# Kernel optimization log

Measured on AMD Instinct MI355X. Metric: run time of the kernel, lower is better.

## Reference

```python
import jax, jax.numpy as jnp
import numpy as np
import math

NUM_BINS = 10
TAIL_BOUND = 5.0
FILTER_CHANNELS = 192
KERNEL_SIZE = 3
N_LAYERS = 3
HALF = 1
MIN_BIN = 1e-3
MIN_DERIV = 1e-3


def conv1d(x, w, b, dilation=1, groups=1, padding=0):
    # x: [B,C,T], w: [O, C//groups, K]
    y = jax.lax.conv_general_dilated(
        x, w, window_strides=(1,), padding=[(padding, padding)],
        rhs_dilation=(dilation,), dimension_numbers=('NCH', 'OIH', 'NCH'),
        feature_group_count=groups)
    return y + b[None, :, None]


def ln_channels(x, g, b, eps=1e-5):
    # LayerNorm over channel dim (VITS modules.LayerNorm)
    m = jnp.mean(x, axis=1, keepdims=True)
    v = jnp.mean((x - m) ** 2, axis=1, keepdims=True)
    return g[None, :, None] * (x - m) * jax.lax.rsqrt(v + eps) + b[None, :, None]


def rq_spline(x1, uw, uh, ud):
    # piecewise rational-quadratic transform with linear tails (Durkan et al.)
    # x1: [B,1,T]; uw,uh: [B,1,T,K]; ud: [B,1,T,K-1]
    K = NUM_BINS
    tb = TAIL_BOUND
    inside = (x1 >= -tb) & (x1 <= tb)

    const = math.log(math.exp(1.0 - MIN_DERIV) - 1.0)  # softplus^-1(1-min_d)
    ud = jnp.pad(ud, [(0, 0)] * (ud.ndim - 1) + [(1, 1)], constant_values=const)

    widths = jax.nn.softmax(uw, axis=-1)
    widths = MIN_BIN + (1.0 - MIN_BIN * K) * widths
    cumw = jnp.pad(jnp.cumsum(widths, -1), [(0, 0)] * (uw.ndim - 1) + [(1, 0)])
    cumw = 2.0 * tb * cumw - tb
    cumw = cumw.at[..., 0].set(-tb).at[..., -1].set(tb)
    widths = cumw[..., 1:] - cumw[..., :-1]

    heights = jax.nn.softmax(uh, axis=-1)
    heights = MIN_BIN + (1.0 - MIN_BIN * K) * heights
    cumh = jnp.pad(jnp.cumsum(heights, -1), [(0, 0)] * (uh.ndim - 1) + [(1, 0)])
    cumh = 2.0 * tb * cumh - tb
    cumh = cumh.at[..., 0].set(-tb).at[..., -1].set(tb)
    heights = cumh[..., 1:] - cumh[..., :-1]

    derivs = MIN_DERIV + jax.nn.softplus(ud)  # [..., K+1]

    xin = jnp.clip(x1, -tb, tb)  # clamp so out-of-range lanes stay finite
    locs = cumw.at[..., -1].add(1e-6)
    bin_idx = jnp.clip(jnp.sum((xin[..., None] >= locs).astype(jnp.int32), -1) - 1, 0, K - 1)

    def take(a):
        return jnp.take_along_axis(a, bin_idx[..., None], axis=-1)[..., 0]

    icw = take(cumw)
    iw = take(widths)
    ich = take(cumh)
    ih = take(heights)
    d_l = take(derivs[..., :-1])
    d_r = take(derivs[..., 1:])
    delta = ih / iw

    theta = (xin - icw) / iw
    t1m = theta * (1.0 - theta)
    numerator = ih * (delta * theta * theta + d_l * t1m)
    denominator = delta + (d_l + d_r - 2.0 * delta) * t1m
    y = ich + numerator / denominator
    dnum = (delta * delta) * (d_r * theta * theta + 2.0 * delta * t1m + d_l * (1.0 - theta) ** 2)
    lad = jnp.log(dnum) - 2.0 * jnp.log(denominator)

    out = jnp.where(inside, y, x1)       # linear tails: identity outside
    lad = jnp.where(inside, lad, 0.0)
    return out, lad


def reference(x, x_mask, pre_w, pre_b, sep_w, sep_b, pw_w, pw_b,
              ln1_g, ln1_b, ln2_g, ln2_b, proj_w, proj_b):
    x0, x1 = x[:, :HALF], x[:, HALF:]
    h = conv1d(x0, pre_w, pre_b)
    # DDSConv (dilated depth-separable conv stack), p_dropout=0
    for i in range(N_LAYERS):
        d = KERNEL_SIZE ** i
        pad = (KERNEL_SIZE * d - d) // 2
        y = conv1d(h * x_mask, sep_w[i], sep_b[i], dilation=d,
                   groups=FILTER_CHANNELS, padding=pad)
        y = jax.nn.gelu(ln_channels(y, ln1_g[i], ln1_b[i]), approximate=False)
        y = conv1d(y, pw_w[i], pw_b[i])
        y = jax.nn.gelu(ln_channels(y, ln2_g[i], ln2_b[i]), approximate=False)
        h = h + y
    h = h * x_mask
    h = conv1d(h, proj_w, proj_b) * x_mask  # [B, half*(3K-1), T]
    b, c, t = x0.shape
    h = h.reshape(b, c, -1, t).transpose(0, 1, 3, 2)  # [B, half, T, 3K-1]
    scale = math.sqrt(FILTER_CHANNELS)
    uw = h[..., :NUM_BINS] / scale
    uh = h[..., NUM_BINS:2 * NUM_BINS] / scale
    ud = h[..., 2 * NUM_BINS:]
    x1o, lad = rq_spline(x1, uw, uh, ud)
    out = jnp.concatenate([x0, x1o], axis=1) * x_mask
    logdet = jnp.sum(lad * x_mask, axis=(1, 2))
    return out, logdet


def setup_inputs() -> dict:
    key = jax.random.key(0)
    ks = jax.random.split(key, 8)
    B, T, C, L, K = 64, 4096, FILTER_CHANNELS, N_LAYERS, KERNEL_SIZE
    return {
        'x': jax.random.normal(ks[0], (B, 2, T), jnp.float32),
        'x_mask': jnp.ones((B, 1, T), jnp.float32),
        'pre_w': jax.random.normal(ks[1], (C, 1, 1), jnp.float32) * 0.1,
        'pre_b': jnp.zeros((C,), jnp.float32),
        'sep_w': jax.random.normal(ks[2], (L, C, 1, K), jnp.float32) * 0.1,
        'sep_b': jnp.zeros((L, C), jnp.float32),
        'pw_w': jax.random.normal(ks[3], (L, C, C, 1), jnp.float32) * (1.0 / np.sqrt(C).astype(np.float32)),
        'pw_b': jnp.zeros((L, C), jnp.float32),
        'ln1_g': jnp.ones((L, C), jnp.float32),
        'ln1_b': jnp.zeros((L, C), jnp.float32),
        'ln2_g': jnp.ones((L, C), jnp.float32),
        'ln2_b': jnp.zeros((L, C), jnp.float32),
        'proj_w': jax.random.normal(ks[4], (HALF * (3 * NUM_BINS - 1), C, 1), jnp.float32) * 0.01,
        'proj_b': jnp.zeros((HALF * (3 * NUM_BINS - 1),), jnp.float32),
    }
```

## Files before the change

kernel.cpp:

```cpp
#include <hip/hip_runtime.h>
#include <stdint.h>

#define TT_ 4096
#define CC_ 192
#define TILE_ 64
#define HALO_ 13
#define TW_ 90
#define HS_ 100
#define YTS_ 200
#define NT_ 512

typedef float f32x2 __attribute__((ext_vector_type(2)));
typedef float f32x4 __attribute__((ext_vector_type(4)));
typedef short s16x4 __attribute__((ext_vector_type(4)));
typedef short s16x8 __attribute__((ext_vector_type(8)));
typedef uint32_t ui32x2 __attribute__((ext_vector_type(2)));
typedef uint32_t ui32x4 __attribute__((ext_vector_type(4)));

__device__ __forceinline__ float bf2f(short s){
  uint32_t u = ((uint32_t)(uint16_t)s) << 16;
  float f; __builtin_memcpy(&f, &u, 4); return f;
}
__device__ __forceinline__ float bfhalf(uint32_t u, int hi){
  uint32_t v = hi ? (u & 0xFFFF0000u) : (u << 16);
  float f; __builtin_memcpy(&f, &v, 4); return f;
}
__device__ __forceinline__ short f2bf(float f){
  uint32_t u; __builtin_memcpy(&u, &f, 4);
  u += 0x7FFFu + ((u >> 16) & 1u);
  return (short)(u >> 16);
}
__device__ __forceinline__ uint32_t fbits(float f){
  uint32_t u; __builtin_memcpy(&u, &f, 4); return u;
}
__device__ __forceinline__ uint32_t pk_trunc(float lo, float hi){
  return __builtin_amdgcn_perm(fbits(hi), fbits(lo), 0x07060302u);
}
__device__ __forceinline__ uint32_t rne_u(float f){
  uint32_t u = fbits(f);
  return u + 0x7FFFu + ((u >> 16) & 1u);
}
__device__ __forceinline__ uint32_t pk_rne(float lo, float hi){
  return __builtin_amdgcn_perm(rne_u(hi), rne_u(lo), 0x07060302u);
}
__device__ __forceinline__ f32x2 pfma(f32x2 a, f32x2 b, f32x2 c){
  return __builtin_elementwise_fma(a, b, c);
}
__device__ __forceinline__ f32x2 gelu2(f32x2 x){
  f32x2 s = x*x;
  f32x2 t = pfma(s, f32x2{0.0713548162f,0.0713548162f}, f32x2{1.5957691216f,1.5957691216f});
  f32x2 p = x*t;
  f32x2 q = p * f32x2{-1.44269504089f,-1.44269504089f};
  f32x2 e; e[0] = __builtin_amdgcn_exp2f(q[0]); e[1] = __builtin_amdgcn_exp2f(q[1]);
  f32x2 d = e + f32x2{1.f,1.f};
  f32x2 r; r[0] = __builtin_amdgcn_rcpf(d[0]); r[1] = __builtin_amdgcn_rcpf(d[1]);
  return x*r;
}
__device__ __forceinline__ int ytix(int row, int col){
  int key = (row ^ (row >> 2)) & 3;
  return row*YTS_ + ((((col >> 3) ^ key) << 3) | (col & 7));
}

template<int D>
__device__ __forceinline__ void dw_pass(const short* __restrict__ Hs, short* __restrict__ YTs,
    const float* __restrict__ sw, const float* __restrict__ sb,
    int jlo, int jhi, int tid){
  constexpr int WO = (D==9) ? 16 : 8;
  constexpr int NU = (D==9) ? 20 : 12;
  for (int g = tid; g < 96*12; g += NT_){
    int cg = g % 96, jg = g / 96;
    int j0 = jg*8;
    if (j0 + 8 <= jlo || j0 >= jhi) continue;
    int c0 = cg*2;
    uint32_t wpa[NU], wpb[NU];
    {
      const uint32_t* ra = (const uint32_t*)(Hs + (c0+0)*HS_ + j0 - WO);
      const uint32_t* rb = (const uint32_t*)(Hs + (c0+1)*HS_ + j0 - WO);
      #pragma unroll
      for (int u = 0; u < NU/2; ++u){
        ui32x2 ta = *(const ui32x2*)(ra + u*2);
        ui32x2 tb = *(const ui32x2*)(rb + u*2);
        wpa[u*2] = ta[0]; wpa[u*2+1] = ta[1];
        wpb[u*2] = tb[0]; wpb[u*2+1] = tb[1];
      }
    }
    f32x2 wv0 = { sw[c0*3+0], sw[c0*3+3] };
    f32x2 wv1 = { sw[c0*3+1], sw[c0*3+4] };
    f32x2 wv2 = { sw[c0*3+2], sw[c0*3+5] };
    f32x2 bb2 = { sb[c0], sb[c0+1] };
    #pragma unroll
    for (int j = 0; j < 8; ++j){
      int h0 = WO + j - D, h1 = WO + j, h2 = WO + j + D;
      f32x2 t0 = { bfhalf(wpa[h0>>1], h0&1), bfhalf(wpb[h0>>1], h0&1) };
      f32x2 t1 = { bfhalf(wpa[h1>>1], h1&1), bfhalf(wpb[h1>>1], h1&1) };
      f32x2 t2 = { bfhalf(wpa[h2>>1], h2&1), bfhalf(wpb[h2>>1], h2&1) };
      f32x2 acc = pfma(wv0, t0, pfma(wv1, t1, pfma(wv2, t2, bb2)));
      *(uint32_t*)(YTs + ytix(j0+j, c0)) = pk_trunc(acc[0], acc[1]);
    }
  }
}

__device__ __forceinline__ void ln_stats(const short* __restrict__ YTs, float* __restrict__ SM,
                                         float* __restrict__ SR, int jlo, int jhi, int tid){
  if (tid < 384){
    int row = tid >> 2, qtr = tid & 3;
    if (row >= jlo && row < jhi){
      f32x2 s2 = {0.f,0.f}, q2 = {0.f,0.f};
      #pragma unroll
      for (int u=0;u<6;++u){
        ui32x4 w = *(const ui32x4*)(YTs + ytix(row, qtr*48 + u*8));
        #pragma unroll
        for (int k=0;k<4;++k){
          f32x2 pr = { bfhalf(w[k],0), bfhalf(w[k],1) };
          s2 += pr; q2 = pfma(pr, pr, q2);
        }
      }
      float s = s2[0]+s2[1], q = q2[0]+q2[1];
      s += __shfl_xor(s,1); q += __shfl_xor(q,1);
      s += __shfl_xor(s,2); q += __shfl_xor(q,2);
      if (qtr==0){
        float mean = s*(1.f/192.f);
        float var = fmaxf(q*(1.f/192.f) - mean*mean, 0.f);
        SM[row]=mean; SR[row]=rsqrtf(var+1e-5f);
      }
    }
  }
}

__global__ __launch_bounds__(512, 4)
void convflow_main(
    const float* __restrict__ x, const float* __restrict__ xmask,
    const float* __restrict__ pre_w, const float* __restrict__ pre_b,
    const float* __restrict__ sep_w, const float* __restrict__ sep_b,
    const float* __restrict__ pw_b,
    const float* __restrict__ ln1_g, const float* __restrict__ ln1_b,
    const float* __restrict__ ln2_g, const float* __restrict__ ln2_b,
    const float* __restrict__ proj_b,
    const short* __restrict__ Wbf, const short* __restrict__ Pbf,
    float* __restrict__ out, float* __restrict__ part)
{
  __shared__ __align__(16) char smem_raw[78592];
  float* MB = (float*)(smem_raw + 0);
  float* XB = (float*)(smem_raw + 640);
  float* SM = (float*)(smem_raw + 1024);
  float* SR = (float*)(smem_raw + 1408);
  short* H  = (short*)(smem_raw + 1792);
  short* YT = (short*)(smem_raw + 40192);
  float* HP = (float*)(smem_raw + 65792);

  const int tid = threadIdx.x;
  const int b = blockIdx.y, tile = blockIdx.x;
  const int t0 = tile*TILE_ - HALO_;

  for (int idx = tid; idx < 160; idx += NT_){
    int j = idx - 16; int t = t0 + j;
    float m = 0.f;
    if (j >= 0 && j < TW_ && t >= 0 && t < TT_) m = xmask[b*TT_ + t];
    MB[idx] = m;
  }
  if (tid < 96){
    int t = t0 + tid; float v = 0.f;
    if (tid < TW_ && t >= 0 && t < TT_) v = x[(b*2)*TT_ + t];
    XB[tid] = v;
  }
  __syncthreads();

  for (int g = tid; g < CC_*24; g += NT_){
    int jq = g % 24, c = g / 24;
    float w = pre_w[c], bb = pre_b[c];
    int j0 = jq*4;
    float v0 = (w*XB[j0+0] + bb)*MB[16+j0+0];
    float v1 = (w*XB[j0+1] + bb)*MB[16+j0+1];
    float v2 = (w*XB[j0+2] + bb)*MB[16+j0+2];
    float v3 = (w*XB[j0+3] + bb)*MB[16+j0+3];
    ui32x2 o; o[0] = pk_rne(v0, v1); o[1] = pk_rne(v2, v3);
    *(ui32x2*)(H + c*HS_ + j0) = o;
  }
  __syncthreads();

  #pragma unroll 1
  for (int li = 0; li < 3; ++li){
    const int jlo = (li==0) ? 1 : ((li==1) ? 4 : 13);
    const int jhi = (li==0) ? 89 : ((li==1) ? 86 : 77);
    const float* sw = sep_w + li*CC_*3;
    const float* sb = sep_b + li*CC_;

    if (li == 0)      dw_pass<1>(H, YT, sw, sb, jlo, jhi, tid);
    else if (li == 1) dw_pass<3>(H, YT, sw, sb, jlo, jhi, tid);
    else              dw_pass<9>(H, YT, sw, sb, jlo, jhi, tid);
    __syncthreads();

    ln_stats(YT, SM, SR, jlo, jhi, tid); __syncthreads();

    {
      const float* g1 = ln1_g + li*CC_;
      const float* b1 = ln1_b + li*CC_;
      for (int g = tid; g < 96*24; g += NT_){
        int ch = g % 24, row = g / 24;
        short* p = YT + ytix(row, ch*8);
        if (row >= jlo && row < jhi){
          float m = SM[row], r = SR[row];
          f32x2 r2 = {r, r}, nm2 = {-m, -m};
          f32x4 ga = *(const f32x4*)&g1[ch*8], gb = *(const f32x4*)&g1[ch*8+4];
          f32x4 ba = *(const f32x4*)&b1[ch*8], bb = *(const f32x4*)&b1[ch*8+4];
          ui32x4 v = *(ui32x4*)p;
          ui32x4 o;
          #pragma unroll
          for (int k=0;k<4;++k){
            f32x2 pr = { bfhalf(v[k],0), bfhalf(v[k],1) };
            f32x2 gk = (k<2) ? f32x2{ga[2*k], ga[2*k+1]} : f32x2{gb[2*k-4], gb[2*k-3]};
            f32x2 bk = (k<2) ? f32x2{ba[2*k], ba[2*k+1]} : f32x2{bb[2*k-4], bb[2*k-3]};
            f32x2 A = gk * r2;
            f32x2 B = pfma(A, nm2, bk);
            f32x2 val = pfma(pr, A, B);
            f32x2 gl = gelu2(val);
            o[k] = pk_trunc(gl[0], gl[1]);
          }
          *(ui32x4*)p = o;
        } else {
          ui32x4 z = {0u,0u,0u,0u};
          *(ui32x4*)p = z;
        }
      }
    }
    __syncthreads();

    {
      int w = tid >> 6, lane = tid & 63, l16 = lane & 15, q = lane >> 4;
      int Mh = w & 3, Nh = w >> 2;
      f32x4 acc[3][3];
      #pragma unroll
      for (int r=0;r<3;r++)
        #pragma unroll
        for (int s=0;s<3;s++){ f32x4 z = {0.f,0.f,0.f,0.f}; acc[r][s] = z; }
      const short* Wl = Wbf + li*CC_*CC_;
      #pragma unroll
      for (int kk=0;kk<6;++kk){
        s16x8 bv[3], av[3];
        #pragma unroll
        for (int s=0;s<3;++s)
          bv[s] = *(const s16x8*)&YT[ytix((Nh*3+s)*16 + l16, kk*32 + q*8)];
        #pragma unroll
        for (int r=0;r<3;++r)
          av[r] = *(const s16x8*)&Wl[((Mh*3+r)*16 + l16)*CC_ + kk*32 + q*8];
        #pragma unroll
        for (int r=0;r<3;++r)
          #pragma unroll
          for (int s=0;s<3;++s)
            acc[r][s] = __builtin_amdgcn_mfma_f32_16x16x32_bf16(av[r], bv[s], acc[r][s], 0, 0, 0);
      }
      __syncthreads();
      #pragma unroll
      for (int r=0;r<3;++r){
        int m0 = (Mh*3+r)*16 + q*4;
        f32x4 bias = *(const f32x4*)&pw_b[li*CC_ + m0];
        #pragma unroll
        for (int s=0;s<3;++s){
          int n = (Nh*3+s)*16 + l16;
          ui32x2 ov;
          ov[0] = pk_trunc(acc[r][s][0]+bias[0], acc[r][s][1]+bias[1]);
          ov[1] = pk_trunc(acc[r][s][2]+bias[2], acc[r][s][3]+bias[3]);
          *(ui32x2*)(YT + ytix(n, m0)) = ov;
        }
      }
      __syncthreads();
    }

    ln_stats(YT, SM, SR, jlo, jhi, tid); __syncthreads();

    {
      const float* g2 = ln2_g + li*CC_;
      const float* b2 = ln2_b + li*CC_;
      for (int g = tid; g < 24*48; g += NT_){
        int jq = g % 24, cq = g / 24;
        int j0 = jq*4, c0 = cq*4;
        if (j0 + 4 <= jlo || j0 >= jhi) continue;
        f32x4 mv = *(f32x4*)&SM[j0], rv = *(f32x4*)&SR[j0];
        f32x4 mk = *(f32x4*)&MB[16 + j0];
        f32x4 gv = *(const f32x4*)&g2[c0], bv = *(const f32x4*)&b2[c0];
        s16x4 yr[4];
        #pragma unroll
        for (int jj=0;jj<4;++jj) yr[jj] = *(s16x4*)(YT + ytix(j0+jj, c0));
        bool ok0 = (j0   >= jlo) && (j0   < jhi);
        bool ok1 = (j0+1 >= jlo) && (j0+1 < jhi);
        bool ok2 = (j0+2 >= jlo) && (j0+2 < jhi);
        bool ok3 = (j0+3 >= jlo) && (j0+3 < jhi);
        #pragma unroll
        for (int cc=0;cc<4;++cc){
          short* hp_ = H + (c0+cc)*HS_ + j0;
          ui32x2 hw = *(ui32x2*)hp_;
          f32x2 gcc = { gv[cc], gv[cc] }, bcc = { bv[cc], bv[cc] };
          ui32x2 ho;
          #pragma unroll
          for (int pp=0; pp<2; ++pp){
            int ja = pp*2, jb = ja+1;
            f32x2 pr = { bf2f(yr[ja][cc]), bf2f(yr[jb][cc]) };
            f32x2 A = f32x2{rv[ja], rv[jb]} * gcc;
            f32x2 B = pfma(A, f32x2{-mv[ja], -mv[jb]}, bcc);
            f32x2 val = pfma(pr, A, B);
            f32x2 gl = gelu2(val);
            f32x2 h2 = { bfhalf(hw[pp],0), bfhalf(hw[pp],1) };
            f32x2 hn = (h2 + gl) * f32x2{mk[ja], mk[jb]};
            bool oa = pp ? ok2 : ok0, ob = pp ? ok3 : ok1;
            float f0 = oa ? hn[0] : h2[0];
            float f1 = ob ? hn[1] : h2[1];
            ho[pp] = pk_rne(f0, f1);
          }
          *(ui32x2*)hp_ = ho;
        }
      }
    }
    __syncthreads();
  }

  {
    int w = tid >> 6;
    if (w < 4){
      int lane = tid & 63, l16 = lane & 15, q = lane >> 4;
      int mt = w >> 1, ntp = w & 1;
      f32x4 pacc[2];
      { f32x4 z = {0.f,0.f,0.f,0.f}; pacc[0] = z; pacc[1] = z; }
      #pragma unroll
      for (int kk=0;kk<6;++kk){
        s16x8 a = *(const s16x8*)&Pbf[(mt*16 + l16)*CC_ + kk*32 + q*8];
        #pragma unroll
        for (int s=0;s<2;++s){
          int n = (ntp*2+s)*16 + l16;
          s16x8 bvv;
          #pragma unroll
          for (int i=0;i<8;++i)
            bvv[i] = H[(kk*32 + q*8 + i)*HS_ + HALO_ + n];
          pacc[s] = __builtin_amdgcn_mfma_f32_16x16x32_bf16(a, bvv, pacc[s], 0, 0, 0);
        }
      }
      #pragma unroll
      for (int s=0;s<2;++s)
        #pragma unroll
        for (int e=0;e<4;e++){
          int m = mt*16 + q*4 + e;
          if (m < 29){
            int n = (ntp*2+s)*16 + l16;
            HP[n*33 + m] = (pacc[s][e] + proj_b[m]) * MB[16 + HALO_ + n];
          }
        }
    }
  }
  __syncthreads();

  if (tid < 64){
    const int n = tid;
    const int tg = tile*TILE_ + n;
    const float msk = MB[16 + HALO_ + n];
    const float* hp = &HP[n*33];
    const float inv_s = 0.07216878364870323f;
    float uw[10], uh[10], ud9[9];
    #pragma unroll
    for (int k=0;k<10;k++){ uw[k] = hp[k]*inv_s; uh[k] = hp[10+k]*inv_s; }
    #pragma unroll
    for (int k=0;k<9;k++) ud9[k] = hp[20+k];

    float cumw[11], cumh[11];
    {
      float mx = uw[0];
      #pragma unroll
      for (int k=1;k<10;k++) mx = fmaxf(mx, uw[k]);
      float ex[10]; float ss = 0.f;
      #pragma unroll
      for (int k=0;k<10;k++){ ex[k] = __expf(uw[k]-mx); ss += ex[k]; }
      float inv = 1.0f/ss;
      cumw[0] = -5.f; float cw = 0.f;
      #pragma unroll
      for (int k=0;k<10;k++){ float wk = 0.001f + 0.99f*(ex[k]*inv); cw += wk; cumw[k+1] = 10.f*cw - 5.f; }
      cumw[10] = 5.f;
    }
    {
      float mx = uh[0];
      #pragma unroll
      for (int k=1;k<10;k++) mx = fmaxf(mx, uh[k]);
      float ex[10]; float ss = 0.f;
      #pragma unroll
      for (int k=0;k<10;k++){ ex[k] = __expf(uh[k]-mx); ss += ex[k]; }
      float inv = 1.0f/ss;
      cumh[0] = -5.f; float ch = 0.f;
      #pragma unroll
      for (int k=0;k<10;k++){ float hk = 0.001f + 0.99f*(ex[k]*inv); ch += hk; cumh[k+1] = 10.f*ch - 5.f; }
      cumh[10] = 5.f;
    }
    float dv[11];
    dv[0] = 1.0f; dv[10] = 1.0f;
    #pragma unroll
    for (int k=0;k<9;k++){
      float u = ud9[k];
      float sp = (u > 15.f) ? u : log1pf(__expf(u));
      dv[k+1] = 0.001f + sp;
    }

    const float x1 = x[(b*2+1)*TT_ + tg];
    const float xin = fminf(fmaxf(x1, -5.f), 5.f);
    int cnt = 0;
    #pragma unroll
    for (int k=0;k<11;k++){
      float lk = cumw[k] + ((k==10) ? 1e-6f : 0.f);
      cnt += (xin >= lk) ? 1 : 0;
    }
    int bin = cnt - 1;
    bin = (bin < 0) ? 0 : ((bin > 9) ? 9 : bin);

    float icw=0.f, iw=1.f, ich=0.f, ih=1.f, dl=1.f, dr=1.f;
    #pragma unroll
    for (int k=0;k<10;k++){
      if (bin == k){
        icw = cumw[k]; iw = cumw[k+1]-cumw[k];
        ich = cumh[k]; ih = cumh[k+1]-cumh[k];
        dl = dv[k]; dr = dv[k+1];
      }
    }
    float delta = ih/iw;
    float th = (xin - icw)/iw;
    float t1m = th*(1.f-th);
    float num = ih*(delta*th*th + dl*t1m);
    float den = delta + (dl + dr - 2.f*delta)*t1m;
    float yv = ich + num/den;
    float omt = 1.f - th;
    float dnum = delta*delta*(dr*th*th + 2.f*delta*t1m + dl*omt*omt);
    float lad = logf(dnum) - 2.f*logf(den);
    bool inside = (x1 >= -5.f) && (x1 <= 5.f);
    float outv = inside ? yv : x1;
    float ladv = inside ? lad : 0.f;

    out[(b*2)*TT_ + tg]   = x[(b*2)*TT_ + tg] * msk;
    out[(b*2+1)*TT_ + tg] = outv * msk;

    float lsum = ladv * msk;
    #pragma unroll
    for (int off = 32; off > 0; off >>= 1) lsum += __shfl_xor(lsum, off);
    if (tid == 0) part[b*64 + tile] = lsum;
  }
}

__global__ void convflow_pre(const float* __restrict__ pw_w, const float* __restrict__ proj_w,
                             short* __restrict__ Wbf, short* __restrict__ Pbf){
  int idx = blockIdx.x*256 + threadIdx.x;
  if (idx < 110592) Wbf[idx] = f2bf(pw_w[idx]);
  if (idx < 32*192){
    int m = idx / 192, k = idx - m*192;
    Pbf[idx] = (m < 29) ? f2bf(proj_w[m*192 + k]) : (short)0;
  }
}

__global__ void convflow_logdet(const float* __restrict__ part, float* __restrict__ out){
  int bb = threadIdx.x;
  if (bb < 64){
    float s = 0.f;
    for (int k=0;k<64;k++) s += part[bb*64 + k];
    out[524288 + bb] = s;
  }
}

extern "C" void kernel_launch(void* const* d_in, const int* in_sizes, int n_in,
                              void* d_out, int out_size, void* d_ws, size_t ws_size,
                              hipStream_t stream) {
  const float* x      = (const float*)d_in[0];
  const float* xmask  = (const float*)d_in[1];
  const float* pre_w  = (const float*)d_in[2];
  const float* pre_b  = (const float*)d_in[3];
  const float* sep_w  = (const float*)d_in[4];
  const float* sep_b  = (const float*)d_in[5];
  const float* pw_w   = (const float*)d_in[6];
  const float* pw_b   = (const float*)d_in[7];
  const float* ln1_g  = (const float*)d_in[8];
  const float* ln1_b  = (const float*)d_in[9];
  const float* ln2_g  = (const float*)d_in[10];
  const float* ln2_b  = (const float*)d_in[11];
  const float* proj_w = (const float*)d_in[12];
  const float* proj_b = (const float*)d_in[13];

  short* Wbf = (short*)d_ws;
  short* Pbf = (short*)((char*)d_ws + 221184);
  float* part = (float*)((char*)d_ws + 233472);
  float* out = (float*)d_out;

  convflow_pre<<<432, 256, 0, stream>>>(pw_w, proj_w, Wbf, Pbf);
  dim3 grid(64, 64);
  convflow_main<<<grid, NT_, 0, stream>>>(x, xmask, pre_w, pre_b, sep_w, sep_b, pw_b,
                                          ln1_g, ln1_b, ln2_g, ln2_b, proj_b,
                                          Wbf, Pbf, out, part);
  convflow_logdet<<<1, 64, 0, stream>>>(part, out);
}
```

Before: 602.7 us.

## Prefetch LDS in LN loops, split spline across thread pairs, parallelize logdet

Several independent changes. The pre-conv now reads x and mask directly from global memory, dropping the XB staging buffer and one barrier. The LN1 and LN2-GELU loops are software-pipelined so the next iteration's LDS loads are issued before the current iteration's math. The spline epilogue is split across thread pairs, one doing the width softmax and bin search and the other the height softmax and softplus derivatives, exchanging values through shuffles, with an added barrier for the two-wave logdet reduction. The logdet kernel now uses 64 blocks with a wave shuffle reduction instead of one serial loop per thread. The trade-off is more registers, extra shuffles, and redundant global loads in the pre-conv.

```diff
diff --git a/kernel.cpp b/kernel.cpp
--- a/kernel.cpp
+++ b/kernel.cpp
@@ -141,7 +141,7 @@
 {
   __shared__ __align__(16) char smem_raw[78592];
   float* MB = (float*)(smem_raw + 0);
-  float* XB = (float*)(smem_raw + 640);
+  float* SP = (float*)(smem_raw + 640);
   float* SM = (float*)(smem_raw + 1024);
   float* SR = (float*)(smem_raw + 1408);
   short* H  = (short*)(smem_raw + 1792);
@@ -158,22 +158,19 @@
     if (j >= 0 && j < TW_ && t >= 0 && t < TT_) m = xmask[b*TT_ + t];
     MB[idx] = m;
   }
-  if (tid < 96){
-    int t = t0 + tid; float v = 0.f;
-    if (tid < TW_ && t >= 0 && t < TT_) v = x[(b*2)*TT_ + t];
-    XB[tid] = v;
-  }
-  __syncthreads();
-
   for (int g = tid; g < CC_*24; g += NT_){
     int jq = g % 24, c = g / 24;
+    int j0 = jq*4;
     float w = pre_w[c], bb = pre_b[c];
-    int j0 = jq*4;
-    float v0 = (w*XB[j0+0] + bb)*MB[16+j0+0];
-    float v1 = (w*XB[j0+1] + bb)*MB[16+j0+1];
-    float v2 = (w*XB[j0+2] + bb)*MB[16+j0+2];
-    float v3 = (w*XB[j0+3] + bb)*MB[16+j0+3];
-    ui32x2 o; o[0] = pk_rne(v0, v1); o[1] = pk_rne(v2, v3);
+    float v[4];
+    #pragma unroll
+    for (int e=0;e<4;e++){
+      int j = j0+e, t = t0+j;
+      float xv = 0.f, mv = 0.f;
+      if (j < TW_ && t >= 0 && t < TT_){ xv = x[(b*2)*TT_ + t]; mv = xmask[b*TT_ + t]; }
+      v[e] = (w*xv + bb)*mv;
+    }
+    ui32x2 o; o[0] = pk_rne(v[0], v[1]); o[1] = pk_rne(v[2], v[3]);
     *(ui32x2*)(H + c*HS_ + j0) = o;
   }
   __syncthreads();
@@ -195,15 +192,24 @@
     {
       const float* g1 = ln1_g + li*CC_;
       const float* b1 = ln1_b + li*CC_;
-      for (int g = tid; g < 96*24; g += NT_){
-        int ch = g % 24, row = g / 24;
-        short* p = YT + ytix(row, ch*8);
+      int g = tid;
+      int ch = g % 24, row = g / 24;
+      short* p = YT + ytix(row, ch*8);
+      ui32x4 v = *(ui32x4*)p;
+      #pragma unroll 1
+      while (g < 2304){
+        int gn = g + NT_;
+        short* pn = p; ui32x4 vn = v; int chn = ch, rown = row;
+        if (gn < 2304){
+          chn = gn % 24; rown = gn / 24;
+          pn = YT + ytix(rown, chn*8);
+          vn = *(ui32x4*)pn;
+        }
         if (row >= jlo && row < jhi){
           float m = SM[row], r = SR[row];
           f32x2 r2 = {r, r}, nm2 = {-m, -m};
           f32x4 ga = *(const f32x4*)&g1[ch*8], gb = *(const f32x4*)&g1[ch*8+4];
           f32x4 ba = *(const f32x4*)&b1[ch*8], bb = *(const f32x4*)&b1[ch*8+4];
-          ui32x4 v = *(ui32x4*)p;
           ui32x4 o;
           #pragma unroll
           for (int k=0;k<4;++k){
@@ -221,6 +227,7 @@
           ui32x4 z = {0u,0u,0u,0u};
           *(ui32x4*)p = z;
         }
+        g = gn; ch = chn; row = rown; p = pn; v = vn;
       }
     }
     __syncthreads();
@@ -271,43 +278,59 @@
     {
       const float* g2 = ln2_g + li*CC_;
       const float* b2 = ln2_b + li*CC_;
-      for (int g = tid; g < 24*48; g += NT_){
-        int jq = g % 24, cq = g / 24;
+      int g = tid;
+      int jq = g % 24, cq = g / 24;
+      s16x4 y0 = *(s16x4*)(YT + ytix(jq*4+0, cq*4));
+      s16x4 y1 = *(s16x4*)(YT + ytix(jq*4+1, cq*4));
+      s16x4 y2 = *(s16x4*)(YT + ytix(jq*4+2, cq*4));
+      s16x4 y3 = *(s16x4*)(YT + ytix(jq*4+3, cq*4));
+      #pragma unroll 1
+      while (g < 1152){
+        int gn = g + NT_;
+        int jqn = jq, cqn = cq;
+        s16x4 y0n = y0, y1n = y1, y2n = y2, y3n = y3;
+        if (gn < 1152){
+          jqn = gn % 24; cqn = gn / 24;
+          y0n = *(s16x4*)(YT + ytix(jqn*4+0, cqn*4));
+          y1n = *(s16x4*)(YT + ytix(jqn*4+1, cqn*4));
+          y2n = *(s16x4*)(YT + ytix(jqn*4+2, cqn*4));
+          y3n = *(s16x4*)(YT + ytix(jqn*4+3, cqn*4));
+        }
         int j0 = jq*4, c0 = cq*4;
-        if (j0 + 4 <= jlo || j0 >= jhi) continue;
-        f32x4 mv = *(f32x4*)&SM[j0], rv = *(f32x4*)&SR[j0];
-        f32x4 mk = *(f32x4*)&MB[16 + j0];
-        f32x4 gv = *(const f32x4*)&g2[c0], bv = *(const f32x4*)&b2[c0];
-        s16x4 yr[4];
-        #pragma unroll
-        for (int jj=0;jj<4;++jj) yr[jj] = *(s16x4*)(YT + ytix(j0+jj, c0));
-        bool ok0 = (j0   >= jlo) && (j0   < jhi);
-        bool ok1 = (j0+1 >= jlo) && (j0+1 < jhi);
-        bool ok2 = (j0+2 >= jlo) && (j0+2 < jhi);
-        bool ok3 = (j0+3 >= jlo) && (j0+3 < jhi);
-        #pragma unroll
-        for (int cc=0;cc<4;++cc){
-          short* hp_ = H + (c0+cc)*HS_ + j0;
-          ui32x2 hw = *(ui32x2*)hp_;
-          f32x2 gcc = { gv[cc], gv[cc] }, bcc = { bv[cc], bv[cc] };
-          ui32x2 ho;
+        if (!(j0 + 4 <= jlo || j0 >= jhi)){
+          f32x4 mv = *(f32x4*)&SM[j0], rv = *(f32x4*)&SR[j0];
+          f32x4 mk = *(f32x4*)&MB[16 + j0];
+          f32x4 gv = *(const f32x4*)&g2[c0], bv = *(const f32x4*)&b2[c0];
+          s16x4 yr[4] = { y0, y1, y2, y3 };
+          bool ok0 = (j0   >= jlo) && (j0   < jhi);
+          bool ok1 = (j0+1 >= jlo) && (j0+1 < jhi);
+          bool ok2 = (j0+2 >= jlo) && (j0+2 < jhi);
+          bool ok3 = (j0+3 >= jlo) && (j0+3 < jhi);
           #pragma unroll
-          for (int pp=0; pp<2; ++pp){
-            int ja = pp*2, jb = ja+1;
-            f32x2 pr = { bf2f(yr[ja][cc]), bf2f(yr[jb][cc]) };
-            f32x2 A = f32x2{rv[ja], rv[jb]} * gcc;
-            f32x2 B = pfma(A, f32x2{-mv[ja], -mv[jb]}, bcc);
-            f32x2 val = pfma(pr, A, B);
-            f32x2 gl = gelu2(val);
-            f32x2 h2 = { bfhalf(hw[pp],0), bfhalf(hw[pp],1) };
-            f32x2 hn = (h2 + gl) * f32x2{mk[ja], mk[jb]};
-            bool oa = pp ? ok2 : ok0, ob = pp ? ok3 : ok1;
-            float f0 = oa ? hn[0] : h2[0];
-            float f1 = ob ? hn[1] : h2[1];
-            ho[pp] = pk_rne(f0, f1);
+          for (int cc=0;cc<4;++cc){
+            short* hp_ = H + (c0+cc)*HS_ + j0;
+            ui32x2 hw = *(ui32x2*)hp_;
+            f32x2 gcc = { gv[cc], gv[cc] }, bcc = { bv[cc], bv[cc] };
+            ui32x2 ho;
+            #pragma unroll
+            for (int pp=0; pp<2; ++pp){
+              int ja = pp*2, jb = ja+1;
+              f32x2 pr = { bf2f(yr[ja][cc]), bf2f(yr[jb][cc]) };
+              f32x2 A = f32x2{rv[ja], rv[jb]} * gcc;
+              f32x2 B = pfma(A, f32x2{-mv[ja], -mv[jb]}, bcc);
+              f32x2 val = pfma(pr, A, B);
+              f32x2 gl = gelu2(val);
+              f32x2 h2 = { bfhalf(hw[pp],0), bfhalf(hw[pp],1) };
+              f32x2 hn = (h2 + gl) * f32x2{mk[ja], mk[jb]};
+              bool oa = pp ? ok2 : ok0, ob = pp ? ok3 : ok1;
+              float f0 = oa ? hn[0] : h2[0];
+              float f1 = ob ? hn[1] : h2[1];
+              ho[pp] = pk_rne(f0, f1);
+            }
+            *(ui32x2*)hp_ = ho;
           }
-          *(ui32x2*)hp_ = ho;
-        }
+        }
+        g = gn; jq = jqn; cq = cqn; y0 = y0n; y1 = y1n; y2 = y2n; y3 = y3n;
       }
     }
     __syncthreads();
@@ -347,95 +370,98 @@
   }
   __syncthreads();
 
-  if (tid < 64){
-    const int n = tid;
+  float lsum_p = 0.f;
+  if (tid < 128){
+    const int n = tid >> 1, half = tid & 1;
     const int tg = tile*TILE_ + n;
     const float msk = MB[16 + HALO_ + n];
     const float* hp = &HP[n*33];
     const float inv_s = 0.07216878364870323f;
-    float uw[10], uh[10], ud9[9];
-    #pragma unroll
-    for (int k=0;k<10;k++){ uw[k] = hp[k]*inv_s; uh[k] = hp[10+k]*inv_s; }
-    #pragma unroll
-    for (int k=0;k<9;k++) ud9[k] = hp[20+k];
-
-    float cumw[11], cumh[11];
+
+    const float x1v = x[(b*2+1)*TT_ + tg];
+    const float xin = fminf(fmaxf(x1v, -5.f), 5.f);
+
+    float cum[11];
     {
-      float mx = uw[0];
-      #pragma unroll
-      for (int k=1;k<10;k++) mx = fmaxf(mx, uw[k]);
+      float u[10];
+      #pragma unroll
+      for (int k=0;k<10;k++) u[k] = hp[half*10 + k]*inv_s;
+      float mx = u[0];
+      #pragma unroll
+      for (int k=1;k<10;k++) mx = fmaxf(mx, u[k]);
       float ex[10]; float ss = 0.f;
       #pragma unroll
-      for (int k=0;k<10;k++){ ex[k] = __expf(uw[k]-mx); ss += ex[k]; }
+      for (int k=0;k<10;k++){ ex[k] = __expf(u[k]-mx); ss += ex[k]; }
       float inv = 1.0f/ss;
-      cumw[0] = -5.f; float cw = 0.f;
-      #pragma unroll
-      for (int k=0;k<10;k++){ float wk = 0.001f + 0.99f*(ex[k]*inv); cw += wk; cumw[k+1] = 10.f*cw - 5.f; }
-      cumw[10] = 5.f;
-    }
-    {
-      float mx = uh[0];
-      #pragma unroll
-      for (int k=1;k<10;k++) mx = fmaxf(mx, uh[k]);
-      float ex[10]; float ss = 0.f;
-      #pragma unroll
-      for (int k=0;k<10;k++){ ex[k] = __expf(uh[k]-mx); ss += ex[k]; }
-      float inv = 1.0f/ss;
-      cumh[0] = -5.f; float ch = 0.f;
-      #pragma unroll
-      for (int k=0;k<10;k++){ float hk = 0.001f + 0.99f*(ex[k]*inv); ch += hk; cumh[k+1] = 10.f*ch - 5.f; }
-      cumh[10] = 5.f;
-    }
+      cum[0] = -5.f; float cw = 0.f;
+      #pragma unroll
+      for (int k=0;k<10;k++){ float wk = 0.001f + 0.99f*(ex[k]*inv); cw += wk; cum[k+1] = 10.f*cw - 5.f; }
+      cum[10] = 5.f;
+    }
+    int bin = 0;
     float dv[11];
-    dv[0] = 1.0f; dv[10] = 1.0f;
-    #pragma unroll
-    for (int k=0;k<9;k++){
-      float u = ud9[k];
-      float sp = (u > 15.f) ? u : log1pf(__expf(u));
-      dv[k+1] = 0.001f + sp;
-    }
-
-    const float x1 = x[(b*2+1)*TT_ + tg];
-    const float xin = fminf(fmaxf(x1, -5.f), 5.f);
-    int cnt = 0;
-    #pragma unroll
-    for (int k=0;k<11;k++){
-      float lk = cumw[k] + ((k==10) ? 1e-6f : 0.f);
-      cnt += (xin >= lk) ? 1 : 0;
-    }
-    int bin = cnt - 1;
-    bin = (bin < 0) ? 0 : ((bin > 9) ? 9 : bin);
-
-    float icw=0.f, iw=1.f, ich=0.f, ih=1.f, dl=1.f, dr=1.f;
-    #pragma unroll
-    for (int k=0;k<10;k++){
-      if (bin == k){
-        icw = cumw[k]; iw = cumw[k+1]-cumw[k];
-        ich = cumh[k]; ih = cumh[k+1]-cumh[k];
-        dl = dv[k]; dr = dv[k+1];
-      }
-    }
-    float delta = ih/iw;
-    float th = (xin - icw)/iw;
-    float t1m = th*(1.f-th);
-    float num = ih*(delta*th*th + dl*t1m);
-    float den = delta + (dl + dr - 2.f*delta)*t1m;
-    float yv = ich + num/den;
-    float omt = 1.f - th;
-    float dnum = delta*delta*(dr*th*th + 2.f*delta*t1m + dl*omt*omt);
-    float lad = logf(dnum) - 2.f*logf(den);
-    bool inside = (x1 >= -5.f) && (x1 <= 5.f);
-    float outv = inside ? yv : x1;
-    float ladv = inside ? lad : 0.f;
-
-    out[(b*2)*TT_ + tg]   = x[(b*2)*TT_ + tg] * msk;
-    out[(b*2+1)*TT_ + tg] = outv * msk;
-
-    float lsum = ladv * msk;
-    #pragma unroll
-    for (int off = 32; off > 0; off >>= 1) lsum += __shfl_xor(lsum, off);
-    if (tid == 0) part[b*64 + tile] = lsum;
-  }
+    if (half == 0){
+      int cnt = 0;
+      #pragma unroll
+      for (int k=0;k<11;k++){
+        float lk = cum[k] + ((k==10) ? 1e-6f : 0.f);
+        cnt += (xin >= lk) ? 1 : 0;
+      }
+      bin = cnt - 1;
+      bin = (bin < 0) ? 0 : ((bin > 9) ? 9 : bin);
+    } else {
+      dv[0] = 1.0f; dv[10] = 1.0f;
+      #pragma unroll
+      for (int k=0;k<9;k++){
+        float u = hp[20+k];
+        float sp = (u > 15.f) ? u : log1pf(__expf(u));
+        dv[k+1] = 0.001f + sp;
+      }
+    }
+    int binx = __shfl_xor(bin, 1);
+    float s0 = 0.f, s1 = 1.f, s2 = 1.f, s3 = 1.f;
+    if (half == 1){
+      bin = binx;
+      #pragma unroll
+      for (int k=0;k<10;k++){
+        if (bin == k){
+          s0 = cum[k]; s1 = cum[k+1]-cum[k];
+          s2 = dv[k];  s3 = dv[k+1];
+        }
+      }
+    } else {
+      #pragma unroll
+      for (int k=0;k<10;k++){
+        if (bin == k){ s0 = cum[k]; s1 = cum[k+1]-cum[k]; }
+      }
+    }
+    float r0 = __shfl_xor(s0,1), r1 = __shfl_xor(s1,1);
+    float r2 = __shfl_xor(s2,1), r3 = __shfl_xor(s3,1);
+    if (half == 0){
+      float icw = s0, iw = s1, ich = r0, ih = r1, dl = r2, dr = r3;
+      float delta = ih/iw;
+      float th = (xin - icw)/iw;
+      float t1m = th*(1.f-th);
+      float num = ih*(delta*th*th + dl*t1m);
+      float den = delta + (dl + dr - 2.f*delta)*t1m;
+      float yv = ich + num/den;
+      float omt = 1.f - th;
+      float dnum = delta*delta*(dr*th*th + 2.f*delta*t1m + dl*omt*omt);
+      float lad = logf(dnum) - 2.f*logf(den);
+      bool inside = (x1v >= -5.f) && (x1v <= 5.f);
+      float outv = inside ? yv : x1v;
+      float ladv = inside ? lad : 0.f;
+      out[(b*2+1)*TT_ + tg] = outv * msk;
+      lsum_p = ladv * msk;
+    } else {
+      out[(b*2)*TT_ + tg] = x[(b*2)*TT_ + tg] * msk;
+    }
+  }
+  #pragma unroll
+  for (int off = 32; off > 0; off >>= 1) lsum_p += __shfl_xor(lsum_p, off);
+  if (tid < 128 && (tid & 63) == 0) SP[tid >> 6] = lsum_p;
+  __syncthreads();
+  if (tid == 0) part[b*64 + tile] = SP[0] + SP[1];
 }
 
 __global__ void convflow_pre(const float* __restrict__ pw_w, const float* __restrict__ proj_w,
@@ -449,12 +475,11 @@
 }
 
 __global__ void convflow_logdet(const float* __restrict__ part, float* __restrict__ out){
-  int bb = threadIdx.x;
-  if (bb < 64){
-    float s = 0.f;
-    for (int k=0;k<64;k++) s += part[bb*64 + k];
-    out[524288 + bb] = s;
-  }
+  int bb = blockIdx.x, k = threadIdx.x;
+  float s = part[bb*64 + k];
+  #pragma unroll
+  for (int off = 32; off > 0; off >>= 1) s += __shfl_xor(s, off);
+  if (k == 0) out[524288 + bb] = s;
 }
 
 extern "C" void kernel_launch(void* const* d_in, const int* in_sizes, int n_in,
@@ -485,5 +510,5 @@
   convflow_main<<<grid, NT_, 0, stream>>>(x, xmask, pre_w, pre_b, sep_w, sep_b, pw_b,
                                           ln1_g, ln1_b, ln2_g, ln2_b, proj_b,
                                           Wbf, Pbf, out, part);
-  convflow_logdet<<<1, 64, 0, stream>>>(part, out);
-}
+  convflow_logdet<<<64, 64, 0, stream>>>(part, out);
+}
```

Measured after the change: 703.2 us. 1.17x slower.
